# Kernel tuning notes

Measured on AMD Instinct MI355X. Metric: run time of the kernel, lower is better.

Reference implementation:

```python
import jax, jax.numpy as jnp
import numpy as np

DN = ('NCHW', 'OIHW', 'NCHW')

def conv2d(x, w, b, stride, pad):
    y = jax.lax.conv_general_dilated(x, w, (stride, stride), [(pad, pad), (pad, pad)], dimension_numbers=DN)
    return y + b[None, :, None, None]

def conv_transpose2d(x, w, b):
    # torch ConvTranspose2d(k=4, stride=2, padding=1): out = (H-1)*2 - 2 + 4 = 2H
    # implemented as input-dilated conv with padding k-1-p = 2 on each side
    y = jax.lax.conv_general_dilated(x, w, (1, 1), [(2, 2), (2, 2)], lhs_dilation=(2, 2), dimension_numbers=DN)
    return y + b[None, :, None, None]

def setup_inputs() -> dict:
    key = jax.random.key(0)
    ks = jax.random.split(key, 8)
    K, D = 512, 128
    x = jax.random.normal(ks[0], (32, 3, 128, 128), jnp.float32)
    ew1 = jax.random.normal(ks[1], (128, 3, 4, 4), jnp.float32) * (1.0 / np.sqrt(3 * 16))
    eb1 = jnp.zeros((128,), jnp.float32)
    ew2 = jax.random.normal(ks[2], (D, 128, 4, 4), jnp.float32) * (1.0 / np.sqrt(128 * 16))
    eb2 = jnp.zeros((D,), jnp.float32)
    E = jax.random.uniform(ks[3], (K, D), jnp.float32, minval=-1.0 / K, maxval=1.0 / K)
    dw1 = jax.random.normal(ks[4], (128, D, 4, 4), jnp.float32) * (1.0 / np.sqrt(D * 16))
    db1 = jnp.zeros((128,), jnp.float32)
    dw2 = jax.random.normal(ks[5], (3, 128, 4, 4), jnp.float32) * (1.0 / np.sqrt(128 * 16))
    db2 = jnp.zeros((3,), jnp.float32)
    return {"x": x, "ew1": ew1, "eb1": eb1, "ew2": ew2, "eb2": eb2, "E": E,
            "dw1": dw1, "db1": db1, "dw2": dw2, "db2": db2}

def reference(x, ew1, eb1, ew2, eb2, E, dw1, db1, dw2, db2):
    # --- encoder: conv stack ---
    h = jax.nn.relu(conv2d(x, ew1, eb1, stride=2, pad=1))       # [B,128,64,64]
    z = conv2d(h, ew2, eb2, stride=2, pad=1)                    # [B,D,32,32] encoder_output
    B, C, H, W = z.shape
    Ze = jnp.transpose(z, (0, 2, 3, 1)).reshape(-1, C)          # [N_e, D], BHWC flattening
    # --- VQ: pairwise sq-dist, argmin, codebook lookup (== one-hot matmul in original) ---
    d = (jnp.sum(Ze * Ze, axis=1, keepdims=True)
         + jnp.sum(E * E, axis=1)
         - 2.0 * jnp.matmul(Ze, E.T))                           # [N_e, K]
    idx = jnp.argmin(d, axis=1)                                 # [N_e]
    Zq = E[idx]                                                 # [N_e, D]
    # faithful to original: Zq_mat.view(encoder_output.shape) with NO permute back
    dec_in = Zq.reshape(B, C, H, W)
    # straight-through estimator
    dec_in = z + jax.lax.stop_gradient(dec_in - z)
    # --- decoder: transposed conv stack ---
    g = jax.nn.relu(conv_transpose2d(dec_in, dw1, db1))         # [B,128,64,64]
    x_recon = jax.nn.sigmoid(conv_transpose2d(g, dw2, db2))     # [B,3,128,128]
    return x_recon
```

## Files before the change

### kernel.cpp

```cpp
#include <hip/hip_runtime.h>
#include <hip/hip_bf16.h>
#include <math.h>


typedef __attribute__((ext_vector_type(8))) short bf16x8;
typedef __attribute__((ext_vector_type(4))) float f32x4;

__device__ __forceinline__ void gload16(const void* g, const void* l) {
    __builtin_amdgcn_global_load_lds(
        (const __attribute__((address_space(1))) void*)g,
        (__attribute__((address_space(3))) void*)l, 16, 0, 0);
}

__device__ __forceinline__ int fragoff(int row, int ks, int lane) {
    return (row << 8) + (((ks << 6) + (lane & 0x30)) ^ ((row & 7) << 4));
}
__device__ __forceinline__ int fragoff64(int row, int ks, int lane) {
    return (row << 7) + (((ks << 6) + (lane & 0x30)) ^ ((row & 7) << 4));
}

__global__ __launch_bounds__(256) void k_init(
    const float* __restrict__ ew1, const float* __restrict__ ew2,
    const float* __restrict__ E,   const float* __restrict__ dw1,
    const float* __restrict__ dw2,
    __hip_bfloat16* __restrict__ hb,  __hip_bfloat16* __restrict__ w2p,
    __hip_bfloat16* __restrict__ w1p, __hip_bfloat16* __restrict__ Ep,
    __hip_bfloat16* __restrict__ w1b, __hip_bfloat16* __restrict__ w2db9,
    __hip_bfloat16* __restrict__ dq,  float* __restrict__ s2)
{
    int bid = blockIdx.x, t = threadIdx.x;
    if (bid < 4160) {
        int tid = bid * 256 + t;
        const int NROW = 32 * 2 * 66 * 128;
        if (tid < NROW) {
            int c = tid & 127;
            int xx = (tid >> 7) % 66;
            int r2 = tid / (66 * 128);
            int yy = (r2 & 1) * 65;
            int n = r2 >> 1;
            hb[((n * 66 + yy) * 66 + xx) * 128 + c] = __float2bfloat16(0.f);
        } else {
            int t2 = tid - NROW;
            int c = t2 & 127;
            int xs = (t2 >> 7) & 1;
            int yy = ((t2 >> 8) & 63) + 1;
            int n = t2 >> 14;
            hb[((n * 66 + yy) * 66 + xs * 65) * 128 + c] = __float2bfloat16(0.f);
        }
    } else if (bid < 5184) {
        int tid = (bid - 4160) * 256 + t;
        int c = tid & 127, o = (tid >> 7) & 127, rs = tid >> 14;
        int r = rs >> 2, s = rs & 3;
        w2p[tid] = __float2bfloat16(ew2[((o * 128 + c) * 4 + r) * 4 + s]);
    } else if (bid < 6208) {
        int tid = (bid - 5184) * 256 + t;
        int c = tid & 127, o = (tid >> 7) & 127, m = tid >> 14;
        int pe = (m >> 3) & 1, qe = (m >> 2) & 1, tt = (m >> 1) & 1, u = m & 1;
        w1p[tid] = __float2bfloat16(dw1[((o * 128 + c) * 4 + (pe + 2 * tt)) * 4 + (qe + 2 * u)]);
    } else if (bid < 6464) {
        int tid = (bid - 6208) * 256 + t;
        Ep[tid] = __float2bfloat16(E[tid]);
    } else if (bid < 6496) {
        int tid = (bid - 6464) * 256 + t;
        int o = tid >> 6, cpos = tid & 63;
        int slot = cpos >> 3, e = cpos & 7;
        int k = ((slot ^ (o & 7)) << 3) | e;
        float v = 0.f;
        if (k < 48) {
            int c = k >> 4, r = (k >> 2) & 3, s = k & 3;
            v = ew1[((o * 3 + c) * 4 + r) * 4 + s];
        }
        w1b[tid] = __float2bfloat16(v);
    } else if (bid < 6568) {
        int tid = (bid - 6496) * 256 + t;
        int cpos = tid & 127;
        int col = (tid >> 7) & 15;
        int de = tid >> 11;
        int o = col & 3, pq = col >> 2;
        int d = de / 3, e_ = de - d * 3;
        int pe = pq >> 1, qe = pq & 1;
        int tt = d - pe, u = e_ - qe;
        float v = 0.f;
        if (o < 3 && tt >= 0 && tt < 2 && u >= 0 && u < 2) {
            int slot = cpos >> 3, el = cpos & 7;
            int csrc = ((slot ^ (col & 7)) << 3) | el;
            v = dw2[((o * 128 + csrc) * 4 + (pe + 2 * tt)) * 4 + (qe + 2 * u)];
        }
        w2db9[tid] = __float2bfloat16(v);
    } else if (bid < 6570) {
        int k = (bid - 6568) * 256 + t;
        float a = 0.f;
        const float* e = E + k * 128;
        for (int c = 0; c < 128; ++c) a = fmaf(e[c], e[c], a);
        s2[k] = a;
    } else {
        int tid = (bid - 6570) * 256 + t;
        int n = tid / 16896;
        int rem = tid - n * 16896;
        int c = rem & 127;
        int pp = rem >> 7;
        int yy, xx;
        if (pp < 68) { yy = (pp >= 34) ? 33 : 0; xx = pp % 34; }
        else { int q = pp - 68; yy = 1 + (q >> 1); xx = (q & 1) * 33; }
        dq[((n * 34 + yy) * 34 + xx) * 128 + c] = __float2bfloat16(0.f);
    }
}

__global__ __launch_bounds__(256) void k_conv1g(
    const float* __restrict__ x, const __hip_bfloat16* __restrict__ w1b,
    const float* __restrict__ b1, __hip_bfloat16* __restrict__ hb)
{
    __shared__ char smem[32768];
    int t = threadIdx.x, lane = t & 63, w = t >> 6;
    int wr = w >> 1, wc = w & 1;
    int bid0 = blockIdx.x;
    int bid = ((bid0 & 7) << 7) | (bid0 >> 3);
    int posbase = bid << 7;

    #pragma unroll
    for (int i = 0; i < 4; ++i)
        gload16(w1b + ((w * 4 + i) * 512 + lane * 8), &smem[16384 + ((w * 4 + i) << 10)]);

    {
        int row = t >> 1, half = t & 1;
        int rowg = posbase + row;
        int n = rowg >> 12, p = (rowg >> 6) & 63, q = rowg & 63;
        #pragma unroll
        for (int j = 0; j < 4; ++j) {
            int d = half * 4 + j;
            int sct = d ^ (row & 7);
            __hip_bfloat16 hv[8];
            #pragma unroll
            for (int e = 0; e < 8; ++e) {
                int k = sct * 8 + e;
                float v = 0.f;
                if (k < 48) {
                    int c = k >> 4, r = (k >> 2) & 3, s4 = k & 3;
                    int y = 2 * p + r - 1, xx = 2 * q + s4 - 1;
                    if (((unsigned)y < 128u) && ((unsigned)xx < 128u))
                        v = x[((n * 3 + c) * 128 + y) * 128 + xx];
                }
                hv[e] = __float2bfloat16(v);
            }
            *(bf16x8*)&smem[(row << 7) + d * 16] = *(bf16x8*)hv;
        }
    }
    __syncthreads();

    f32x4 acc[4][4];
    #pragma unroll
    for (int mi = 0; mi < 4; ++mi)
        #pragma unroll
        for (int ni = 0; ni < 4; ++ni) acc[mi][ni] = (f32x4){0.f, 0.f, 0.f, 0.f};

    #pragma unroll
    for (int ks = 0; ks < 2; ++ks) {
        bf16x8 av[4], bv[4];
        #pragma unroll
        for (int mi = 0; mi < 4; ++mi)
            av[mi] = *(const bf16x8*)&smem[fragoff64((wr << 6) + (mi << 4) + (lane & 15), ks, lane)];
        #pragma unroll
        for (int ni = 0; ni < 4; ++ni)
            bv[ni] = *(const bf16x8*)&smem[16384 + fragoff64((wc << 6) + (ni << 4) + (lane & 15), ks, lane)];
        #pragma unroll
        for (int mi = 0; mi < 4; ++mi)
            #pragma unroll
            for (int ni = 0; ni < 4; ++ni)
                acc[mi][ni] = __builtin_amdgcn_mfma_f32_16x16x32_bf16(av[mi], bv[ni], acc[mi][ni], 0, 0, 0);
    }

    int rg = (lane >> 4) << 2;
    #pragma unroll
    for (int mi = 0; mi < 4; ++mi)
        #pragma unroll
        for (int ni = 0; ni < 4; ++ni) {
            int o = (wc << 6) + (ni << 4) + (lane & 15);
            float bias = b1[o];
            #pragma unroll
            for (int j = 0; j < 4; ++j) {
                int rowg = posbase + (wr << 6) + (mi << 4) + rg + j;
                int n = rowg >> 12, p = (rowg >> 6) & 63, q = rowg & 63;
                float v = acc[mi][ni][j] + bias;
                v = v > 0.f ? v : 0.f;
                hb[((n * 66 + p + 1) * 66 + q + 1) * 128 + o] = __float2bfloat16(v);
            }
        }
}

__global__ __launch_bounds__(256) void k_conv2vq(
    const __hip_bfloat16* __restrict__ hb, const __hip_bfloat16* __restrict__ w2p,
    const float* __restrict__ b2, const __hip_bfloat16* __restrict__ Ep,
    const float* __restrict__ s2, __hip_bfloat16* __restrict__ dq)
{
    __shared__ char smem[32768];
    int t = threadIdx.x, lane = t & 63, w = t >> 6;
    int bid0 = blockIdx.x;
    int bid = ((bid0 & 7) << 6) | (bid0 >> 3);
    int posbase = bid << 6;
    int n = posbase >> 10, p0 = (posbase >> 5) & 31;

    int aoff[2];
    #pragma unroll
    for (int i = 0; i < 2; ++i) {
        int r = ((w << 1) + i) * 8 + (lane >> 3);
        int slot = lane & 7;
        int p = p0 + (r >> 5), q = r & 31;
        aoff[i] = (((n * 66 + 2 * p) * 66 + 2 * q) << 7) + ((slot ^ (r & 7)) << 3);
    }
    int boff[4];
    #pragma unroll
    for (int i = 0; i < 4; ++i) {
        int o = ((w << 2) + i) * 8 + (lane >> 3);
        int slot = lane & 7;
        boff[i] = (o << 7) + ((slot ^ (o & 7)) << 3);
    }

    f32x4 acc[4][2];
    #pragma unroll
    for (int mi = 0; mi < 4; ++mi)
        #pragma unroll
        for (int ni = 0; ni < 2; ++ni) acc[mi][ni] = (f32x4){0.f, 0.f, 0.f, 0.f};

    for (int step = 0; step < 32; ++step) {
        int rs = step >> 1, ch = step & 1;
        int aadd = ((((rs >> 2) * 66) + (rs & 3)) << 7) + (ch << 6);
        int badd = (rs << 14) + (ch << 6);
        __syncthreads();
        #pragma unroll
        for (int i = 0; i < 2; ++i)
            gload16(hb + aoff[i] + aadd, &smem[((w << 1) + i) << 10]);
        #pragma unroll
        for (int i = 0; i < 4; ++i)
            gload16(w2p + boff[i] + badd, &smem[16384 + (((w << 2) + i) << 10)]);
        __syncthreads();
        #pragma unroll
        for (int ks = 0; ks < 2; ++ks) {
            bf16x8 av[4], bv[2];
            #pragma unroll
            for (int mi = 0; mi < 4; ++mi)
                av[mi] = *(const bf16x8*)&smem[fragoff64((mi << 4) + (lane & 15), ks, lane)];
            #pragma unroll
            for (int ni = 0; ni < 2; ++ni)
                bv[ni] = *(const bf16x8*)&smem[16384 + fragoff64((w << 5) + (ni << 4) + (lane & 15), ks, lane)];
            #pragma unroll
            for (int mi = 0; mi < 4; ++mi)
                #pragma unroll
                for (int ni = 0; ni < 2; ++ni)
                    acc[mi][ni] = __builtin_amdgcn_mfma_f32_16x16x32_bf16(av[mi], bv[ni], acc[mi][ni], 0, 0, 0);
        }
    }

    __syncthreads();
    {
        int rg = (lane >> 4) << 2;
        #pragma unroll
        for (int mi = 0; mi < 4; ++mi)
            #pragma unroll
            for (int ni = 0; ni < 2; ++ni) {
                int o = (w << 5) + (ni << 4) + (lane & 15);
                float bias = b2[o];
                #pragma unroll
                for (int j = 0; j < 4; ++j) {
                    int r = (mi << 4) + rg + j;
                    int byteoff = (r << 8) + (((((o >> 3) ^ (r & 7))) << 4) | ((o & 7) << 1));
                    __hip_bfloat16 hv = __float2bfloat16(acc[mi][ni][j] + bias);
                    *(__hip_bfloat16*)&smem[byteoff] = hv;
                }
            }
    }
    __syncthreads();

    float bvv[4][4];
    int   bii[4][4];
    #pragma unroll
    for (int mi = 0; mi < 4; ++mi)
        #pragma unroll
        for (int j = 0; j < 4; ++j) { bvv[mi][j] = 3.4e38f; bii[mi][j] = 0; }

    for (int chunk = 0; chunk < 8; ++chunk) {
        __syncthreads();
        #pragma unroll
        for (int i = 0; i < 4; ++i) {
            int kl = (((w << 2) + i) << 2) + (lane >> 4);
            int slot = lane & 15;
            gload16(Ep + ((((chunk << 6) + kl) << 7) + ((slot ^ (kl & 7)) << 3)),
                    &smem[16384 + (((w << 2) + i) << 10)]);
        }
        __syncthreads();
        f32x4 a2[4];
        #pragma unroll
        for (int mi = 0; mi < 4; ++mi) a2[mi] = (f32x4){0.f, 0.f, 0.f, 0.f};
        #pragma unroll
        for (int ks = 0; ks < 4; ++ks) {
            bf16x8 av[4], bv;
            #pragma unroll
            for (int mi = 0; mi < 4; ++mi)
                av[mi] = *(const bf16x8*)&smem[fragoff((mi << 4) + (lane & 15), ks, lane)];
            bv = *(const bf16x8*)&smem[16384 + fragoff((w << 4) + (lane & 15), ks, lane)];
            #pragma unroll
            for (int mi = 0; mi < 4; ++mi)
                a2[mi] = __builtin_amdgcn_mfma_f32_16x16x32_bf16(av[mi], bv, a2[mi], 0, 0, 0);
        }
        int kg = (chunk << 6) + (w << 4) + (lane & 15);
        float s2v = s2[kg];
        #pragma unroll
        for (int mi = 0; mi < 4; ++mi)
            #pragma unroll
            for (int j = 0; j < 4; ++j) {
                float sc = s2v - 2.f * a2[mi][j];
                if (sc < bvv[mi][j]) { bvv[mi][j] = sc; bii[mi][j] = kg; }
            }
    }

    __syncthreads();
    float* redv  = (float*)&smem[16384];
    int*   redi  = (int*)&smem[16384 + 1024];
    int*   idx_l = (int*)&smem[16384 + 2048];
    #pragma unroll
    for (int mi = 0; mi < 4; ++mi)
        #pragma unroll
        for (int j = 0; j < 4; ++j) {
            float v = bvv[mi][j];
            int   ix = bii[mi][j];
            #pragma unroll
            for (int m = 1; m < 16; m <<= 1) {
                float ov = __shfl_xor(v, m, 64);
                int   oi = __shfl_xor(ix, m, 64);
                if (ov < v || (ov == v && oi < ix)) { v = ov; ix = oi; }
            }
            if ((lane & 15) == 0) {
                int r = (mi << 4) + ((lane >> 4) << 2) + j;
                redv[(r << 2) + w] = v;
                redi[(r << 2) + w] = ix;
            }
        }
    __syncthreads();
    if (t < 64) {
        float bv_ = redv[t << 2];
        int   bi_ = redi[t << 2];
        #pragma unroll
        for (int w2 = 1; w2 < 4; ++w2) {
            float ov = redv[(t << 2) + w2];
            int   oi = redi[(t << 2) + w2];
            if (ov < bv_ || (ov == bv_ && oi < bi_)) { bv_ = ov; bi_ = oi; }
        }
        idx_l[t] = bi_;
    }
    __syncthreads();

    #pragma unroll
    for (int i = 0; i < 4; ++i) {
        int idx2 = (w << 2) + i;
        int r = (idx2 << 2) + (lane >> 4);
        int krow = idx_l[r];
        gload16(Ep + ((krow << 7) + ((lane & 15) << 3)), &smem[idx2 << 10]);
    }
    __syncthreads();

    int cd0 = (posbase >> 3) & 127;
    const unsigned short* eb = (const unsigned short*)smem;
    #pragma unroll
    for (int k2 = 0; k2 < 4; ++k2) {
        int sp = (k2 << 8) + t;
        int hi = sp >> 7, lo = sp & 127;
        int y = sp >> 5, xx = sp & 31;
        unsigned short vals[8];
        #pragma unroll
        for (int ci = 0; ci < 8; ++ci)
            vals[ci] = eb[(((ci << 3) + hi) << 7) + lo];
        __hip_bfloat16* dst = dq + ((n * 34 + y + 1) * 34 + (xx + 1)) * 128 + cd0;
        *(bf16x8*)dst = *(bf16x8*)vals;
    }
}

__global__ __launch_bounds__(256) void k_deconv1(
    const __hip_bfloat16* __restrict__ dq, const __hip_bfloat16* __restrict__ w1p,
    const float* __restrict__ b1, __hip_bfloat16* __restrict__ g)
{
    __shared__ char smem[32768];
    int t = threadIdx.x, lane = t & 63, w = t >> 6;
    int wr = w >> 1, wc = w & 1;
    int bid0 = blockIdx.x;
    int bid = ((bid0 & 7) << 7) | (bid0 >> 3);
    int ag = bid & 7, qe = (bid >> 3) & 1, pe = (bid >> 4) & 1, n = bid >> 5;

    int aoff[4], boff[4];
    #pragma unroll
    for (int i = 0; i < 4; ++i) {
        int r = ((w << 2) + i) * 8 + (lane >> 3);
        int slot = lane & 7;
        int a = (ag << 2) + (r >> 5), b = r & 31;
        aoff[i] = (((n * 34 + (a + pe)) * 34 + (b + qe)) << 7) + ((slot ^ (r & 7)) << 3);
        boff[i] = (r << 7) + ((slot ^ (r & 7)) << 3);
    }

    f32x4 acc[4][4];
    #pragma unroll
    for (int mi = 0; mi < 4; ++mi)
        #pragma unroll
        for (int ni = 0; ni < 4; ++ni) acc[mi][ni] = (f32x4){0.f, 0.f, 0.f, 0.f};

    int mbase = (pe << 3) | (qe << 2);
    for (int step = 0; step < 8; ++step) {
        int tu = step >> 1, ch = step & 1;
        int tt = tu >> 1, u = tu & 1;
        int aadd = ((tt * 34 + u) << 7) + (ch << 6);
        int badd = ((mbase + tu) << 14) + (ch << 6);
        __syncthreads();
        #pragma unroll
        for (int i = 0; i < 4; ++i) {
            gload16(dq + aoff[i] + aadd, &smem[((w << 2) + i) << 10]);
            gload16(w1p + boff[i] + badd, &smem[16384 + (((w << 2) + i) << 10)]);
        }
        __syncthreads();
        #pragma unroll
        for (int ks = 0; ks < 2; ++ks) {
            bf16x8 av[4], bv[4];
            #pragma unroll
            for (int mi = 0; mi < 4; ++mi)
                av[mi] = *(const bf16x8*)&smem[fragoff64((wr << 6) + (mi << 4) + (lane & 15), ks, lane)];
            #pragma unroll
            for (int ni = 0; ni < 4; ++ni)
                bv[ni] = *(const bf16x8*)&smem[16384 + fragoff64((wc << 6) + (ni << 4) + (lane & 15), ks, lane)];
            #pragma unroll
            for (int mi = 0; mi < 4; ++mi)
                #pragma unroll
                for (int ni = 0; ni < 4; ++ni)
                    acc[mi][ni] = __builtin_amdgcn_mfma_f32_16x16x32_bf16(av[mi], bv[ni], acc[mi][ni], 0, 0, 0);
        }
    }

    int rg = (lane >> 4) << 2;
    #pragma unroll
    for (int mi = 0; mi < 4; ++mi)
        #pragma unroll
        for (int ni = 0; ni < 4; ++ni) {
            int o = (wc << 6) + (ni << 4) + (lane & 15);
            float bias = b1[o];
            #pragma unroll
            for (int j = 0; j < 4; ++j) {
                int row = (wr << 6) + (mi << 4) + rg + j;
                int a = (ag << 2) + (row >> 5), b = row & 31;
                int y = 2 * a + pe, xx2 = 2 * b + qe;
                float v = acc[mi][ni][j] + bias;
                v = v > 0.f ? v : 0.f;
                g[((n * 66 + y + 1) * 66 + xx2 + 1) * 128 + o] = __float2bfloat16(v);
            }
        }
}

__global__ __launch_bounds__(256) void k_deconv2g(
    const __hip_bfloat16* __restrict__ g, const __hip_bfloat16* __restrict__ w2db9,
    const float* __restrict__ b2, float* __restrict__ out)
{
    __shared__ char smem[36864];
    int t = threadIdx.x, lane = t & 63, w = t >> 6;
    int bid0 = blockIdx.x;
    int bid = ((bid0 & 7) << 7) | (bid0 >> 3);
    int atile = bid & 31, n = bid >> 5;
    int a0 = atile << 1;

    int aoff[8];
    #pragma unroll
    for (int i = 0; i < 8; ++i) {
        int row = (((w << 3) + i) << 2) + (lane >> 4);
        int al = row >> 6, b = row & 63;
        int csw = ((lane & 15) ^ (row & 7)) << 3;
        aoff[i] = (((n * 66 + (a0 + al)) * 66 + b) << 7) + csw;
    }

    f32x4 acc[2];
    acc[0] = (f32x4){0.f, 0.f, 0.f, 0.f};
    acc[1] = (f32x4){0.f, 0.f, 0.f, 0.f};

    for (int de = 0; de < 9; ++de) {
        __syncthreads();
        int dy = de / 3, dx = de - dy * 3;
        int tapoff = ((dy * 66 + dx) << 7);
        #pragma unroll
        for (int i = 0; i < 8; ++i)
            gload16(g + aoff[i] + tapoff, &smem[((w << 3) + i) << 10]);
        gload16(w2db9 + (de << 11) + (w << 9) + (lane << 3), &smem[32768 + (w << 10)]);
        __syncthreads();
        #pragma unroll
        for (int ks = 0; ks < 4; ++ks) {
            bf16x8 av[2], bv;
            #pragma unroll
            for (int mi = 0; mi < 2; ++mi)
                av[mi] = *(const bf16x8*)&smem[fragoff((w << 5) + (mi << 4) + (lane & 15), ks, lane)];
            bv = *(const bf16x8*)&smem[32768 + fragoff(lane & 15, ks, lane)];
            #pragma unroll
            for (int mi = 0; mi < 2; ++mi)
                acc[mi] = __builtin_amdgcn_mfma_f32_16x16x32_bf16(av[mi], bv, acc[mi], 0, 0, 0);
        }
    }

    int rg = (lane >> 4) << 2;
    int col = lane & 15, o = col & 3, pq = col >> 2;
    if (o < 3) {
        int pe = pq >> 1, qe = pq & 1;
        float bias = b2[o];
        #pragma unroll
        for (int mi = 0; mi < 2; ++mi)
            #pragma unroll
            for (int j = 0; j < 4; ++j) {
                int row = (w << 5) + (mi << 4) + rg + j;
                int y = 2 * (a0 + (row >> 6)) + pe;
                int x = 2 * (row & 63) + qe;
                float v = acc[mi][j] + bias;
                out[((n * 3 + o) * 128 + y) * 128 + x] = 1.f / (1.f + expf(-v));
            }
    }
}

extern "C" void kernel_launch(void* const* d_in, const int* in_sizes, int n_in,
                              void* d_out, int out_size, void* d_ws, size_t ws_size,
                              hipStream_t stream) {
    const float* x   = (const float*)d_in[0];
    const float* ew1 = (const float*)d_in[1];
    const float* eb1 = (const float*)d_in[2];
    const float* ew2 = (const float*)d_in[3];
    const float* eb2 = (const float*)d_in[4];
    const float* E   = (const float*)d_in[5];
    const float* dw1 = (const float*)d_in[6];
    const float* db1 = (const float*)d_in[7];
    const float* dw2 = (const float*)d_in[8];
    const float* db2 = (const float*)d_in[9];
    float* out = (float*)d_out;

    char* W = (char*)d_ws;
    __hip_bfloat16* hb    = (__hip_bfloat16*)(W + 0);
    __hip_bfloat16* g     = (__hip_bfloat16*)(W + 0);
    __hip_bfloat16* dq    = (__hip_bfloat16*)(W + 75497472);
    __hip_bfloat16* w2p   = (__hip_bfloat16*)(W + 84967424);
    __hip_bfloat16* w1p   = (__hip_bfloat16*)(W + 85491712);
    __hip_bfloat16* Ep    = (__hip_bfloat16*)(W + 86016000);
    __hip_bfloat16* w2db9 = (__hip_bfloat16*)(W + 86147072);
    float*          s2    = (float*)(W + 86184192);
    __hip_bfloat16* w1b   = (__hip_bfloat16*)(W + 86186240);

    k_init    <<<8682, 256, 0, stream>>>(ew1, ew2, E, dw1, dw2,
                                         hb, w2p, w1p, Ep, w1b, w2db9, dq, s2);
    k_conv1g  <<<1024, 256, 0, stream>>>(x, w1b, eb1, hb);
    k_conv2vq <<<512,  256, 0, stream>>>(hb, w2p, eb2, Ep, s2, dq);
    k_deconv1 <<<1024, 256, 0, stream>>>(dq, w1p, db1, g);
    k_deconv2g<<<1024, 256, 0, stream>>>(g, w2db9, db2, out);
}
```

Before: 119.7 us.

## Double-buffer LDS staging in conv/VQ/deconv kernels and stage input rows for conv1

Converts the K-loops of conv2vq, the VQ codebook scan, deconv1 and deconv2 into double-buffered LDS pipelines. The next stage's global_load_lds is issued before computing on the current buffer, so each iteration needs one barrier instead of two. Deconv2 is re-chunked into 18 half-K steps with a matching swizzle, and its weight packing drops the pre-swizzle. conv1 now stages the needed input rows into LDS with async loads instead of gathering scattered global reads per element. LDS use per block grows, which may reduce occupancy.

```diff
diff --git a/kernel.cpp b/kernel.cpp
--- a/kernel.cpp
+++ b/kernel.cpp
@@ -73,7 +73,7 @@
         w1b[tid] = __float2bfloat16(v);
     } else if (bid < 6568) {
         int tid = (bid - 6496) * 256 + t;
-        int cpos = tid & 127;
+        int c = tid & 127;
         int col = (tid >> 7) & 15;
         int de = tid >> 11;
         int o = col & 3, pq = col >> 2;
@@ -81,11 +81,8 @@
         int pe = pq >> 1, qe = pq & 1;
         int tt = d - pe, u = e_ - qe;
         float v = 0.f;
-        if (o < 3 && tt >= 0 && tt < 2 && u >= 0 && u < 2) {
-            int slot = cpos >> 3, el = cpos & 7;
-            int csrc = ((slot ^ (col & 7)) << 3) | el;
-            v = dw2[((o * 128 + csrc) * 4 + (pe + 2 * tt)) * 4 + (qe + 2 * u)];
-        }
+        if (o < 3 && tt >= 0 && tt < 2 && u >= 0 && u < 2)
+            v = dw2[((o * 128 + c) * 4 + (pe + 2 * tt)) * 4 + (qe + 2 * u)];
         w2db9[tid] = __float2bfloat16(v);
     } else if (bid < 6570) {
         int k = (bid - 6568) * 256 + t;
@@ -110,21 +107,35 @@
     const float* __restrict__ x, const __hip_bfloat16* __restrict__ w1b,
     const float* __restrict__ b1, __hip_bfloat16* __restrict__ hb)
 {
-    __shared__ char smem[32768];
+    __shared__ char smem[41984];
     int t = threadIdx.x, lane = t & 63, w = t >> 6;
     int wr = w >> 1, wc = w & 1;
     int bid0 = blockIdx.x;
     int bid = ((bid0 & 7) << 7) | (bid0 >> 3);
     int posbase = bid << 7;
+    int ng = posbase >> 12, p0g = (posbase >> 6) & 63;
 
     #pragma unroll
     for (int i = 0; i < 4; ++i)
         gload16(w1b + ((w * 4 + i) * 512 + lane * 8), &smem[16384 + ((w * 4 + i) << 10)]);
 
+    #pragma unroll
+    for (int k3 = 0; k3 < 3; ++k3) {
+        int j = w + (k3 << 2);
+        if (j < 9) {
+            int wrow = (j << 1) | (lane >> 5);
+            int c = wrow / 6, yy = wrow - c * 6;
+            int y = 2 * p0g - 1 + yy;
+            int ysrc = y < 0 ? 0 : (y > 127 ? 127 : y);
+            gload16(x + (((ng * 3 + c) * 128 + ysrc) << 7) + ((lane & 31) << 2),
+                    &smem[32768 + (j << 10)]);
+        }
+    }
+    __syncthreads();
+
     {
         int row = t >> 1, half = t & 1;
-        int rowg = posbase + row;
-        int n = rowg >> 12, p = (rowg >> 6) & 63, q = rowg & 63;
+        int pl = row >> 6, q = row & 63;
         #pragma unroll
         for (int j = 0; j < 4; ++j) {
             int d = half * 4 + j;
@@ -136,9 +147,12 @@
                 float v = 0.f;
                 if (k < 48) {
                     int c = k >> 4, r = (k >> 2) & 3, s4 = k & 3;
-                    int y = 2 * p + r - 1, xx = 2 * q + s4 - 1;
-                    if (((unsigned)y < 128u) && ((unsigned)xx < 128u))
-                        v = x[((n * 3 + c) * 128 + y) * 128 + xx];
+                    int y = 2 * (p0g + pl) + r - 1;
+                    int xg = 2 * q + s4 - 1;
+                    if (((unsigned)y < 128u) && ((unsigned)xg < 128u)) {
+                        int wrow = c * 6 + 2 * pl + r;
+                        v = *(const float*)&smem[32768 + (wrow << 9) + (xg << 2)];
+                    }
                 }
                 hv[e] = __float2bfloat16(v);
             }
@@ -192,7 +206,7 @@
     const float* __restrict__ b2, const __hip_bfloat16* __restrict__ Ep,
     const float* __restrict__ s2, __hip_bfloat16* __restrict__ dq)
 {
-    __shared__ char smem[32768];
+    __shared__ char smem[49152];
     int t = threadIdx.x, lane = t & 63, w = t >> 6;
     int bid0 = blockIdx.x;
     int bid = ((bid0 & 7) << 6) | (bid0 >> 3);
@@ -215,42 +229,54 @@
         boff[i] = (o << 7) + ((slot ^ (o & 7)) << 3);
     }
 
+#define C2_STAGE(STEP, BASE) { \
+    int rs_ = (STEP) >> 1, ch_ = (STEP) & 1; \
+    int aadd_ = ((((rs_ >> 2) * 66) + (rs_ & 3)) << 7) + (ch_ << 6); \
+    int badd_ = (rs_ << 14) + (ch_ << 6); \
+    _Pragma("unroll") \
+    for (int i = 0; i < 2; ++i) \
+        gload16(hb + aoff[i] + aadd_, &smem[(BASE) + (((w << 1) + i) << 10)]); \
+    _Pragma("unroll") \
+    for (int i = 0; i < 4; ++i) \
+        gload16(w2p + boff[i] + badd_, &smem[(BASE) + 8192 + (((w << 2) + i) << 10)]); }
+
     f32x4 acc[4][2];
     #pragma unroll
     for (int mi = 0; mi < 4; ++mi)
         #pragma unroll
         for (int ni = 0; ni < 2; ++ni) acc[mi][ni] = (f32x4){0.f, 0.f, 0.f, 0.f};
 
+    C2_STAGE(0, 0);
+    __syncthreads();
     for (int step = 0; step < 32; ++step) {
-        int rs = step >> 1, ch = step & 1;
-        int aadd = ((((rs >> 2) * 66) + (rs & 3)) << 7) + (ch << 6);
-        int badd = (rs << 14) + (ch << 6);
-        __syncthreads();
-        #pragma unroll
-        for (int i = 0; i < 2; ++i)
-            gload16(hb + aoff[i] + aadd, &smem[((w << 1) + i) << 10]);
-        #pragma unroll
-        for (int i = 0; i < 4; ++i)
-            gload16(w2p + boff[i] + badd, &smem[16384 + (((w << 2) + i) << 10)]);
-        __syncthreads();
+        int cb = (step & 1) * 24576;
+        if (step < 31) C2_STAGE(step + 1, ((step + 1) & 1) * 24576);
         #pragma unroll
         for (int ks = 0; ks < 2; ++ks) {
             bf16x8 av[4], bv[2];
             #pragma unroll
             for (int mi = 0; mi < 4; ++mi)
-                av[mi] = *(const bf16x8*)&smem[fragoff64((mi << 4) + (lane & 15), ks, lane)];
+                av[mi] = *(const bf16x8*)&smem[cb + fragoff64((mi << 4) + (lane & 15), ks, lane)];
             #pragma unroll
             for (int ni = 0; ni < 2; ++ni)
-                bv[ni] = *(const bf16x8*)&smem[16384 + fragoff64((w << 5) + (ni << 4) + (lane & 15), ks, lane)];
+                bv[ni] = *(const bf16x8*)&smem[cb + 8192 + fragoff64((w << 5) + (ni << 4) + (lane & 15), ks, lane)];
             #pragma unroll
             for (int mi = 0; mi < 4; ++mi)
                 #pragma unroll
                 for (int ni = 0; ni < 2; ++ni)
                     acc[mi][ni] = __builtin_amdgcn_mfma_f32_16x16x32_bf16(av[mi], bv[ni], acc[mi][ni], 0, 0, 0);
         }
-    }
-
-    __syncthreads();
+        __syncthreads();
+    }
+
+#define VQ_STAGE(CHUNK, BASE) { \
+    _Pragma("unroll") \
+    for (int i = 0; i < 4; ++i) { \
+        int kl_ = (((w << 2) + i) << 2) + (lane >> 4); \
+        gload16(Ep + ((((CHUNK) << 6) + kl_) << 7) + (((lane & 15) ^ (kl_ & 7)) << 3), \
+                &smem[(BASE) + (((w << 2) + i) << 10)]); \
+    } }
+
     {
         int rg = (lane >> 4) << 2;
         #pragma unroll
@@ -268,6 +294,7 @@
                 }
             }
     }
+    VQ_STAGE(0, 16384);
     __syncthreads();
 
     float bvv[4][4];
@@ -278,15 +305,8 @@
         for (int j = 0; j < 4; ++j) { bvv[mi][j] = 3.4e38f; bii[mi][j] = 0; }
 
     for (int chunk = 0; chunk < 8; ++chunk) {
-        __syncthreads();
-        #pragma unroll
-        for (int i = 0; i < 4; ++i) {
-            int kl = (((w << 2) + i) << 2) + (lane >> 4);
-            int slot = lane & 15;
-            gload16(Ep + ((((chunk << 6) + kl) << 7) + ((slot ^ (kl & 7)) << 3)),
-                    &smem[16384 + (((w << 2) + i) << 10)]);
-        }
-        __syncthreads();
+        int eb = 16384 + ((chunk & 1) << 14);
+        if (chunk < 7) VQ_STAGE(chunk + 1, 16384 + (((chunk + 1) & 1) << 14));
         f32x4 a2[4];
         #pragma unroll
         for (int mi = 0; mi < 4; ++mi) a2[mi] = (f32x4){0.f, 0.f, 0.f, 0.f};
@@ -296,7 +316,7 @@
             #pragma unroll
             for (int mi = 0; mi < 4; ++mi)
                 av[mi] = *(const bf16x8*)&smem[fragoff((mi << 4) + (lane & 15), ks, lane)];
-            bv = *(const bf16x8*)&smem[16384 + fragoff((w << 4) + (lane & 15), ks, lane)];
+            bv = *(const bf16x8*)&smem[eb + fragoff((w << 4) + (lane & 15), ks, lane)];
             #pragma unroll
             for (int mi = 0; mi < 4; ++mi)
                 a2[mi] = __builtin_amdgcn_mfma_f32_16x16x32_bf16(av[mi], bv, a2[mi], 0, 0, 0);
@@ -310,9 +330,9 @@
                 float sc = s2v - 2.f * a2[mi][j];
                 if (sc < bvv[mi][j]) { bvv[mi][j] = sc; bii[mi][j] = kg; }
             }
-    }
-
-    __syncthreads();
+        __syncthreads();
+    }
+
     float* redv  = (float*)&smem[16384];
     int*   redi  = (int*)&smem[16384 + 1024];
     int*   idx_l = (int*)&smem[16384 + 2048];
@@ -358,7 +378,7 @@
     __syncthreads();
 
     int cd0 = (posbase >> 3) & 127;
-    const unsigned short* eb = (const unsigned short*)smem;
+    const unsigned short* eb2p = (const unsigned short*)smem;
     #pragma unroll
     for (int k2 = 0; k2 < 4; ++k2) {
         int sp = (k2 << 8) + t;
@@ -367,7 +387,7 @@
         unsigned short vals[8];
         #pragma unroll
         for (int ci = 0; ci < 8; ++ci)
-            vals[ci] = eb[(((ci << 3) + hi) << 7) + lo];
+            vals[ci] = eb2p[(((ci << 3) + hi) << 7) + lo];
         __hip_bfloat16* dst = dq + ((n * 34 + y + 1) * 34 + (xx + 1)) * 128 + cd0;
         *(bf16x8*)dst = *(bf16x8*)vals;
     }
@@ -377,7 +397,7 @@
     const __hip_bfloat16* __restrict__ dq, const __hip_bfloat16* __restrict__ w1p,
     const float* __restrict__ b1, __hip_bfloat16* __restrict__ g)
 {
-    __shared__ char smem[32768];
+    __shared__ char smem[65536];
     int t = threadIdx.x, lane = t & 63, w = t >> 6;
     int wr = w >> 1, wc = w & 1;
     int bid0 = blockIdx.x;
@@ -393,6 +413,18 @@
         aoff[i] = (((n * 34 + (a + pe)) * 34 + (b + qe)) << 7) + ((slot ^ (r & 7)) << 3);
         boff[i] = (r << 7) + ((slot ^ (r & 7)) << 3);
     }
+    int mbase = (pe << 3) | (qe << 2);
+
+#define D1_STAGE(STEP, BASE) { \
+    int tu_ = (STEP) >> 1, ch_ = (STEP) & 1; \
+    int tt_ = tu_ >> 1, u_ = tu_ & 1; \
+    int aadd_ = ((tt_ * 34 + u_) << 7) + (ch_ << 6); \
+    int badd_ = ((mbase + tu_) << 14) + (ch_ << 6); \
+    _Pragma("unroll") \
+    for (int i = 0; i < 4; ++i) { \
+        gload16(dq + aoff[i] + aadd_, &smem[(BASE) + (((w << 2) + i) << 10)]); \
+        gload16(w1p + boff[i] + badd_, &smem[(BASE) + 16384 + (((w << 2) + i) << 10)]); \
+    } }
 
     f32x4 acc[4][4];
     #pragma unroll
@@ -400,34 +432,27 @@
         #pragma unroll
         for (int ni = 0; ni < 4; ++ni) acc[mi][ni] = (f32x4){0.f, 0.f, 0.f, 0.f};
 
-    int mbase = (pe << 3) | (qe << 2);
+    D1_STAGE(0, 0);
+    __syncthreads();
     for (int step = 0; step < 8; ++step) {
-        int tu = step >> 1, ch = step & 1;
-        int tt = tu >> 1, u = tu & 1;
-        int aadd = ((tt * 34 + u) << 7) + (ch << 6);
-        int badd = ((mbase + tu) << 14) + (ch << 6);
-        __syncthreads();
-        #pragma unroll
-        for (int i = 0; i < 4; ++i) {
-            gload16(dq + aoff[i] + aadd, &smem[((w << 2) + i) << 10]);
-            gload16(w1p + boff[i] + badd, &smem[16384 + (((w << 2) + i) << 10)]);
-        }
-        __syncthreads();
+        int cb = (step & 1) * 32768;
+        if (step < 7) D1_STAGE(step + 1, ((step + 1) & 1) * 32768);
         #pragma unroll
         for (int ks = 0; ks < 2; ++ks) {
             bf16x8 av[4], bv[4];
             #pragma unroll
             for (int mi = 0; mi < 4; ++mi)
-                av[mi] = *(const bf16x8*)&smem[fragoff64((wr << 6) + (mi << 4) + (lane & 15), ks, lane)];
+                av[mi] = *(const bf16x8*)&smem[cb + fragoff64((wr << 6) + (mi << 4) + (lane & 15), ks, lane)];
             #pragma unroll
             for (int ni = 0; ni < 4; ++ni)
-                bv[ni] = *(const bf16x8*)&smem[16384 + fragoff64((wc << 6) + (ni << 4) + (lane & 15), ks, lane)];
+                bv[ni] = *(const bf16x8*)&smem[cb + 16384 + fragoff64((wc << 6) + (ni << 4) + (lane & 15), ks, lane)];
             #pragma unroll
             for (int mi = 0; mi < 4; ++mi)
                 #pragma unroll
                 for (int ni = 0; ni < 4; ++ni)
                     acc[mi][ni] = __builtin_amdgcn_mfma_f32_16x16x32_bf16(av[mi], bv[ni], acc[mi][ni], 0, 0, 0);
         }
+        __syncthreads();
     }
 
     int rg = (lane >> 4) << 2;
@@ -460,39 +485,48 @@
     int atile = bid & 31, n = bid >> 5;
     int a0 = atile << 1;
 
-    int aoff[8];
-    #pragma unroll
-    for (int i = 0; i < 8; ++i) {
-        int row = (((w << 3) + i) << 2) + (lane >> 4);
-        int al = row >> 6, b = row & 63;
-        int csw = ((lane & 15) ^ (row & 7)) << 3;
-        aoff[i] = (((n * 66 + (a0 + al)) * 66 + b) << 7) + csw;
-    }
+    int aoff[4];
+    #pragma unroll
+    for (int i = 0; i < 4; ++i) {
+        int r = ((w << 2) + i) * 8 + (lane >> 3);
+        int al = r >> 6, b = r & 63;
+        aoff[i] = (((n * 66 + (a0 + al)) * 66 + b) << 7) + (((lane & 7) ^ (r & 7)) << 3);
+    }
+
+#define D2_STAGE(STEP, BASE) { \
+    int de_ = (STEP) >> 1, ch_ = (STEP) & 1; \
+    int dy_ = de_ / 3, dx_ = de_ - dy_ * 3; \
+    int aadd_ = ((dy_ * 66 + dx_) << 7) + (ch_ << 6); \
+    _Pragma("unroll") \
+    for (int i = 0; i < 4; ++i) \
+        gload16(g + aoff[i] + aadd_, &smem[(BASE) + (((w << 2) + i) << 10)]); \
+    if (w < 2) { \
+        int kl_ = (w << 3) + (lane >> 3); \
+        gload16(w2db9 + (de_ << 11) + (kl_ << 7) + (ch_ << 6) + (((lane & 7) ^ (kl_ & 7)) << 3), \
+                &smem[(BASE) + 16384 + (w << 10)]); \
+    } }
 
     f32x4 acc[2];
     acc[0] = (f32x4){0.f, 0.f, 0.f, 0.f};
     acc[1] = (f32x4){0.f, 0.f, 0.f, 0.f};
 
-    for (int de = 0; de < 9; ++de) {
-        __syncthreads();
-        int dy = de / 3, dx = de - dy * 3;
-        int tapoff = ((dy * 66 + dx) << 7);
-        #pragma unroll
-        for (int i = 0; i < 8; ++i)
-            gload16(g + aoff[i] + tapoff, &smem[((w << 3) + i) << 10]);
-        gload16(w2db9 + (de << 11) + (w << 9) + (lane << 3), &smem[32768 + (w << 10)]);
-        __syncthreads();
-        #pragma unroll
-        for (int ks = 0; ks < 4; ++ks) {
+    D2_STAGE(0, 0);
+    __syncthreads();
+    for (int step = 0; step < 18; ++step) {
+        int cb = (step & 1) * 18432;
+        if (step < 17) D2_STAGE(step + 1, ((step + 1) & 1) * 18432);
+        #pragma unroll
+        for (int ks = 0; ks < 2; ++ks) {
             bf16x8 av[2], bv;
             #pragma unroll
             for (int mi = 0; mi < 2; ++mi)
-                av[mi] = *(const bf16x8*)&smem[fragoff((w << 5) + (mi << 4) + (lane & 15), ks, lane)];
-            bv = *(const bf16x8*)&smem[32768 + fragoff(lane & 15, ks, lane)];
+                av[mi] = *(const bf16x8*)&smem[cb + fragoff64((w << 5) + (mi << 4) + (lane & 15), ks, lane)];
+            bv = *(const bf16x8*)&smem[cb + 16384 + fragoff64(lane & 15, ks, lane)];
             #pragma unroll
             for (int mi = 0; mi < 2; ++mi)
                 acc[mi] = __builtin_amdgcn_mfma_f32_16x16x32_bf16(av[mi], bv, acc[mi], 0, 0, 0);
         }
+        __syncthreads();
     }
 
     int rg = (lane >> 4) << 2;
```

After: 112.5 us. -6.0%, faster.
